# Kernel tuning notes

Measured on AMD Instinct MI355X. Metric: run time of the kernel, lower is better.

The kernel has to match this reference:

```python
import jax, jax.numpy as jnp
import numpy as np

NUM_CLASSES = 80
TOPK = 9
EPS_OVERLAPS = 1e-6  # mmdet BboxOverlaps2D: union clamped to eps
EPS_YOLOV6 = 1e-9    # yolov6_iou_calculator: eps added to union


def _pairwise_iou(b1, b2, eps, add_eps):
    # b1: (..., M, 4), b2: (..., N, 4) xyxy -> (..., M, N)
    lt = jnp.maximum(b1[..., :, None, :2], b2[..., None, :, :2])
    rb = jnp.minimum(b1[..., :, None, 2:], b2[..., None, :, 2:])
    wh = jnp.clip(rb - lt, 0.0)
    overlap = wh[..., 0] * wh[..., 1]
    a1 = (b1[..., 2] - b1[..., 0]) * (b1[..., 3] - b1[..., 1])
    a2 = (b2[..., 2] - b2[..., 0]) * (b2[..., 3] - b2[..., 1])
    union = a1[..., :, None] + a2[..., None, :] - overlap
    return overlap / (union + eps) if add_eps else overlap / jnp.maximum(union, eps)


def _assign(pred_bboxes, priors, gt_labels, gt_bboxes, pad_bbox_flag, num_level_priors):
    num_level_priors = tuple(int(n) for n in np.asarray(num_level_priors))
    # priors (x, y, stride_w, stride_h) -> 5*stride cell boxes in xyxy
    cell_half = priors[:, 2:] * 2.5
    prior_boxes = jnp.concatenate([priors[:, :2] - cell_half, priors[:, :2] + cell_half], axis=-1)
    bs, num_gt = gt_bboxes.shape[0], gt_bboxes.shape[1]
    num_priors = priors.shape[0]
    gt_flat = gt_bboxes.reshape(-1, 4)

    # step 1: IoU between all priors and all gts
    overlaps = _pairwise_iou(gt_flat, prior_boxes, EPS_OVERLAPS, False).reshape(bs, num_gt, num_priors)

    # step 2: center distances
    gt_cxy = (gt_flat[:, :2] + gt_flat[:, 2:]) * 0.5
    prior_cxy = (prior_boxes[:, :2] + prior_boxes[:, 2:]) * 0.5
    dist = jnp.sqrt(jnp.sum((gt_cxy[:, None, :] - prior_cxy[None, :, :]) ** 2, axis=-1))
    dist = dist.reshape(bs, num_gt, num_priors)

    # step 3: per-level topk closest candidates
    pad_bool = pad_bbox_flag[..., 0] > 0  # (bs, num_gt)
    b_ix = jnp.arange(bs)[:, None, None]
    g_ix = jnp.arange(num_gt)[None, :, None]
    is_in_list, cand_list = [], []
    start = 0
    for pl in num_level_priors:
        k = min(TOPK, pl)
        d_l = jax.lax.dynamic_slice_in_dim(dist, start, pl, axis=-1)
        _, idx = jax.lax.top_k(-d_l, k)  # (bs, num_gt, k) smallest distances
        cand_list.append(idx + start)
        idx_m = jnp.where(pad_bool[..., None], idx, 0)
        counts = jnp.zeros((bs, num_gt, pl), dist.dtype).at[b_ix, g_ix, idx_m].add(1.0)
        is_in_list.append(jnp.where(counts > 1, jnp.zeros_like(counts), counts))
        start += pl
    is_in_candidate = jnp.concatenate(is_in_list, axis=-1)   # (bs, num_gt, num_priors)
    candidate_idxs = jnp.concatenate(cand_list, axis=-1)     # (bs, num_gt, k*levels)

    # step 4: mean + std of candidate IoUs as threshold
    candidate_overlaps = jnp.where(is_in_candidate > 0, overlaps, jnp.zeros_like(overlaps))
    gathered = jnp.take_along_axis(candidate_overlaps, candidate_idxs, axis=-1)
    thr = jnp.mean(gathered, axis=-1, keepdims=True) + jnp.std(gathered, axis=-1, keepdims=True, ddof=1)

    # step 5: keep candidates above threshold
    is_pos = jnp.where(candidate_overlaps > thr, is_in_candidate, jnp.zeros_like(is_in_candidate))

    # step 6: center of prior must lie inside gt box
    lt = prior_cxy[None, None, :, :] - gt_bboxes[:, :, None, :2]
    rb = gt_bboxes[:, :, None, 2:] - prior_cxy[None, None, :, :]
    is_in_gts = (jnp.minimum(lt, rb).min(axis=-1) > 1e-9).astype(gt_bboxes.dtype)

    pos_mask = is_pos * is_in_gts * pad_bbox_flag  # pad flag broadcasts (bs,num_gt,1)

    # resolve priors assigned to multiple gts: keep highest IoU gt
    fg = pos_mask.sum(axis=-2)  # (bs, num_priors)
    best_gt = jnp.argmax(overlaps, axis=1)  # (bs, num_priors)
    is_max = jax.nn.one_hot(best_gt, num_gt, dtype=pos_mask.dtype).transpose(0, 2, 1)
    pos_mask = jnp.where(fg[:, None, :] > 1, is_max, pos_mask)
    fg_mask = pos_mask.sum(axis=-2)                 # (bs, num_priors)
    gt_idx = jnp.argmax(pos_mask, axis=-2)          # (bs, num_priors)

    # targets
    flat_idx = gt_idx + jnp.arange(bs)[:, None] * num_gt
    assigned_labels = gt_labels.reshape(-1)[flat_idx]
    assigned_labels = jnp.where(fg_mask > 0, assigned_labels, NUM_CLASSES)
    assigned_bboxes = gt_bboxes.reshape(-1, 4)[flat_idx]
    assigned_scores = jax.nn.one_hot(assigned_labels, NUM_CLASSES + 1, dtype=gt_bboxes.dtype)[..., :NUM_CLASSES]

    # weight scores by IoU with predictions
    ious = _pairwise_iou(gt_bboxes, pred_bboxes, EPS_YOLOV6, True) * pos_mask
    assigned_scores = assigned_scores * jnp.max(ious, axis=-2)[..., None]
    return assigned_labels, assigned_bboxes, assigned_scores, fg_mask > 0


def setup_inputs() -> dict:
    key = jax.random.key(0)
    k0, k1, k2, k3, k4 = jax.random.split(key, 5)
    bs, num_gt, img = 32, 64, 640
    strides = (8, 16, 32)
    pri = []
    for s in strides:
        n = img // s
        xs = (np.arange(n, dtype=np.float32) + 0.5) * s
        gy, gx = np.meshgrid(xs, xs, indexing='ij')
        pts = np.stack([gx.ravel(), gy.ravel()], axis=1)
        st = np.full((pts.shape[0], 2), s, dtype=np.float32)
        pri.append(np.concatenate([pts, st], axis=1))
    priors = jnp.asarray(np.concatenate(pri, axis=0))  # (8400, 4)
    num_level_priors = (6400, 1600, 400)
    num_priors = priors.shape[0]
    cxy = jax.random.uniform(k0, (bs, num_gt, 2), minval=50.0, maxval=590.0)
    wh = jax.random.uniform(k1, (bs, num_gt, 2), minval=20.0, maxval=200.0)
    gt_bboxes = jnp.concatenate([cxy - wh * 0.5, cxy + wh * 0.5], axis=-1)
    gt_labels = jax.random.randint(k2, (bs, num_gt, 1), 0, NUM_CLASSES)
    pad_bbox_flag = jnp.ones((bs, num_gt, 1), jnp.float32)
    pcxy = priors[None, :, :2] + jax.random.normal(k3, (bs, num_priors, 2)) * 4.0
    pwh = jax.random.uniform(k4, (bs, num_priors, 2), minval=10.0, maxval=150.0)
    pred_bboxes = jnp.concatenate([pcxy - pwh * 0.5, pcxy + pwh * 0.5], axis=-1)
    return {'pred_bboxes': pred_bboxes, 'priors': priors, 'gt_labels': gt_labels,
            'gt_bboxes': gt_bboxes, 'pad_bbox_flag': pad_bbox_flag,
            'num_level_priors': num_level_priors}


def reference(pred_bboxes, priors, gt_labels, gt_bboxes, pad_bbox_flag, num_level_priors):
    return _assign(pred_bboxes, priors, gt_labels, gt_bboxes, pad_bbox_flag, num_level_priors)
```

## Files before the change

### kernel.cpp

```cpp
#include <hip/hip_runtime.h>

#define BS 32
#define NG 64
#define NP 8400
#define NTOPK 9
#define NUM_CLASSES 80
#define NCAND 27

__device__ __forceinline__ unsigned long long wave_min_u64(unsigned long long k) {
    #pragma unroll
    for (int off = 1; off < 64; off <<= 1) {
        unsigned long long o = __shfl_xor(k, off, 64);
        k = (o < k) ? o : k;
    }
    return k;
}

__global__ __launch_bounds__(256) void k_candidates(
    const float4* __restrict__ gt_bboxes,
    const float*  __restrict__ pad_flag,
    unsigned long long* __restrict__ posbits
) {
    const int bg   = (blockIdx.x * 256 + threadIdx.x) >> 6;
    const int lane = threadIdx.x & 63;
    const int b  = bg >> 6;
    const int g  = bg & 63;

    const float4 gt  = gt_bboxes[bg];
    const float  pad = pad_flag[bg];
    const float  gcx = (gt.x + gt.z) * 0.5f;
    const float  gcy = (gt.y + gt.w) * 0.5f;
    const float  garea = (gt.z - gt.x) * (gt.w - gt.y);

    const float lvl_s[3] = {8.0f, 16.0f, 32.0f};
    const int   lvl_n[3] = {80, 40, 20};
    const int   lvl_b[3] = {0, 6400, 8000};

    float ov[NCAND];
    int   ixs[NCAND];

    float sum = 0.0f;

    const int dy5 = lane / 5;
    const int dx5 = lane - dy5 * 5;

    #pragma unroll
    for (int L = 0; L < 3; ++L) {
        const float s    = lvl_s[L];
        const int   n    = lvl_n[L];
        const int   base = lvl_b[L];

        int wx = (int)floorf(gcx / s) - 2;
        int wy = (int)floorf(gcy / s) - 2;
        wx = min(max(wx, 0), n - 5);
        wy = min(max(wy, 0), n - 5);

        unsigned long long key = ~0ull;
        if (lane < 25) {
            const int   iy  = wy + dy5;
            const int   ix  = wx + dx5;
            const float py  = ((float)iy + 0.5f) * s;
            const float px  = ((float)ix + 0.5f) * s;
            const float ddx = gcx - px;
            const float ddy = gcy - py;
            const float d   = sqrtf(ddx * ddx + ddy * ddy);
            key = ((unsigned long long)__float_as_uint(d) << 32) |
                  (unsigned int)(base + iy * n + ix);
        }

        const float hx = s * 2.5f;
        #pragma unroll
        for (int q = 0; q < NTOPK; ++q) {
            const unsigned long long m = wave_min_u64(key);
            if (key == m) key = ~0ull;

            const int slot = L * NTOPK + q;
            const int idx  = (int)(m & 0xffffffffu);
            const int rel  = idx - base;
            const int iy   = rel / n;
            const int ix   = rel - iy * n;
            const float px = ((float)ix + 0.5f) * s;
            const float py = ((float)iy + 0.5f) * s;
            const float px0 = px - hx, py0 = py - hx;
            const float px1 = px + hx, py1 = py + hx;
            float lx = fmaxf(gt.x, px0), ly = fmaxf(gt.y, py0);
            float rx = fminf(gt.z, px1), ry = fminf(gt.w, py1);
            float w = fmaxf(rx - lx, 0.0f), h = fmaxf(ry - ly, 0.0f);
            float ovl = w * h;
            float parea = (px1 - px0) * (py1 - py0);
            float o = ovl / fmaxf(garea + parea - ovl, 1e-6f);
            ov[slot]  = o;
            ixs[slot] = idx;
            sum += o;
        }
    }

    const float mean = sum / (float)NCAND;
    float var = 0.0f;
    #pragma unroll
    for (int i = 0; i < NCAND; ++i) {
        float d = ov[i] - mean;
        var += d * d;
    }
    const float thr = mean + sqrtf(var / (float)(NCAND - 1));

    if (pad > 0.0f && lane == 0) {
        #pragma unroll
        for (int i = 0; i < NCAND; ++i) {
            if (ov[i] > thr) {
                const int   L    = i / NTOPK;
                const float s    = lvl_s[L];
                const int   n    = lvl_n[L];
                const int   base = lvl_b[L];
                const int idx = ixs[i];
                const int rel = idx - base;
                const int iy  = rel / n;
                const int ix  = rel - iy * n;
                const float px = ((float)ix + 0.5f) * s;
                const float py = ((float)iy + 0.5f) * s;
                float mm = fminf(fminf(px - gt.x, py - gt.y),
                                 fminf(gt.z - px, gt.w - py));
                if (mm > 1e-9f) {
                    atomicOr(&posbits[(size_t)b * NP + idx], 1ull << g);
                }
            }
        }
    }
}

__global__ __launch_bounds__(256) void k_assign(
    const float4* __restrict__ priors,
    const float4* __restrict__ gt_bboxes,
    const int*    __restrict__ gt_labels,
    const float4* __restrict__ pred_bboxes,
    const unsigned long long* __restrict__ posbits,
    float* __restrict__ out)
{
    __shared__ float4 s_gt[NG];
    __shared__ int    s_lab[NG];
    __shared__ int    s_plab[256];
    __shared__ float  s_piou[256];

    const int b   = blockIdx.y;
    const int tid = threadIdx.x;
    if (tid < NG) {
        s_gt[tid]  = gt_bboxes[b * NG + tid];
        s_lab[tid] = gt_labels[b * NG + tid];
    }
    __syncthreads();

    const int p0 = blockIdx.x * 256;
    const int p  = p0 + tid;
    int   label  = NUM_CLASSES;
    float iou_w  = 0.0f;

    if (p < NP) {
        const size_t bp = (size_t)b * NP + p;
        unsigned long long mask = posbits[bp];
        int fg = __popcll(mask);
        int gidx = 0;

        if (fg > 1) {
            float4 pr = priors[p];
            float hx = pr.z * 2.5f, hy = pr.w * 2.5f;
            float px0 = pr.x - hx, py0 = pr.y - hy, px1 = pr.x + hx, py1 = pr.y + hy;
            float parea = (px1 - px0) * (py1 - py0);
            float best = -1.0f;
            for (int gg = 0; gg < NG; ++gg) {
                float4 gtb = s_gt[gg];
                float lx = fmaxf(gtb.x, px0), ly = fmaxf(gtb.y, py0);
                float rx = fminf(gtb.z, px1), ry = fminf(gtb.w, py1);
                float w = fmaxf(rx - lx, 0.0f), h = fmaxf(ry - ly, 0.0f);
                float ovl = w * h;
                float ga = (gtb.z - gtb.x) * (gtb.w - gtb.y);
                float v = ovl / fmaxf(ga + parea - ovl, 1e-6f);
                if (v > best) { best = v; gidx = gg; }
            }
        } else if (fg == 1) {
            gidx = __ffsll((unsigned long long)mask) - 1;
        }

        const bool  fgm = fg > 0;
        const float4 gtb = s_gt[gidx];
        label = fgm ? s_lab[gidx] : NUM_CLASSES;

        if (fgm) {
            float4 pb = pred_bboxes[bp];
            float lx = fmaxf(gtb.x, pb.x), ly = fmaxf(gtb.y, pb.y);
            float rx = fminf(gtb.z, pb.z), ry = fminf(gtb.w, pb.w);
            float w = fmaxf(rx - lx, 0.0f), h = fmaxf(ry - ly, 0.0f);
            float ov = w * h;
            float ga = (gtb.z - gtb.x) * (gtb.w - gtb.y);
            float pa = (pb.z - pb.x) * (pb.w - pb.y);
            iou_w = ov / (ga + pa - ov + 1e-9f);
        }

        out[bp] = (float)label;
        ((float4*)(out + (size_t)BS * NP))[bp] = gtb;
        out[(size_t)BS * NP * 85 + bp] = fgm ? 1.0f : 0.0f;
    }

    s_plab[tid] = label;
    s_piou[tid] = iou_w;
    __syncthreads();

    const int npr  = min(256, NP - p0);
    const int nfl4 = npr * 20;
    float4* o4 = (float4*)(out + (size_t)BS * NP * 5 + ((size_t)b * NP + p0) * 80);
    for (int q = tid; q < nfl4; q += 256) {
        int pl   = q / 20;
        int comp = q - pl * 20;
        int lab  = s_plab[pl];
        float iw = s_piou[pl];
        int dd = lab - comp * 4;
        float4 v;
        v.x = (dd == 0) ? iw : 0.0f;
        v.y = (dd == 1) ? iw : 0.0f;
        v.z = (dd == 2) ? iw : 0.0f;
        v.w = (dd == 3) ? iw : 0.0f;
        o4[q] = v;
    }
}

extern "C" void kernel_launch(void* const* d_in, const int* in_sizes, int n_in,
                              void* d_out, int out_size, void* d_ws, size_t ws_size,
                              hipStream_t stream) {
    const float4* pred_bboxes = (const float4*)d_in[0];
    const float4* priors      = (const float4*)d_in[1];
    const int*    gt_labels   = (const int*)d_in[2];
    const float4* gt_bboxes   = (const float4*)d_in[3];
    const float*  pad_flag    = (const float*)d_in[4];

    unsigned long long* posbits = (unsigned long long*)d_ws;
    hipMemsetAsync(posbits, 0, (size_t)BS * NP * sizeof(unsigned long long), stream);

    k_candidates<<<dim3(BS * NG * 64 / 256), dim3(256), 0, stream>>>(
        gt_bboxes, pad_flag, posbits);

    k_assign<<<dim3((NP + 255) / 256, BS), dim3(256), 0, stream>>>(
        priors, gt_bboxes, gt_labels, pred_bboxes, posbits, (float*)d_out);
}
```

Before: 129.4 us.

## Zero score tensor with memset and scatter sparse foreground scores via compacted list

The dense 80-class score tensor is no longer written element by element inside the assign kernel. It is cleared with hipMemsetAsync, and the assign kernel appends (index, label, iou) entries for foreground priors to a compacted list through an atomic counter. A new scatter kernel then writes only those nonzero scores. Separately, the candidate top-k reduction now shuffles over only 32 lanes, since just 25 lanes hold valid keys. The aim is to use the DMA/fill path for the large zero write and drop the per-element selects, at the cost of an extra kernel launch, a global atomic, and a second memset.

After: 147.3 us. 13.9% more time.

```diff
diff --git a/kernel.cpp b/kernel.cpp
--- a/kernel.cpp
+++ b/kernel.cpp
@@ -6,10 +6,13 @@
 #define NTOPK 9
 #define NUM_CLASSES 80
 #define NCAND 27
-
-__device__ __forceinline__ unsigned long long wave_min_u64(unsigned long long k) {
+#define MAXENT (BS * NG * NCAND)
+
+#define POSBYTES ((size_t)BS * NP * 8)
+
+__device__ __forceinline__ unsigned long long wave_min_u64_32(unsigned long long k) {
     #pragma unroll
-    for (int off = 1; off < 64; off <<= 1) {
+    for (int off = 1; off < 32; off <<= 1) {
         unsigned long long o = __shfl_xor(k, off, 64);
         k = (o < k) ? o : k;
     }
@@ -71,7 +74,7 @@
         const float hx = s * 2.5f;
         #pragma unroll
         for (int q = 0; q < NTOPK; ++q) {
-            const unsigned long long m = wave_min_u64(key);
+            const unsigned long long m = wave_min_u64_32(key);
             if (key == m) key = ~0ull;
 
             const int slot = L * NTOPK + q;
@@ -134,12 +137,12 @@
     const int*    __restrict__ gt_labels,
     const float4* __restrict__ pred_bboxes,
     const unsigned long long* __restrict__ posbits,
+    unsigned int* __restrict__ counter,
+    uint2*        __restrict__ entries,
     float* __restrict__ out)
 {
     __shared__ float4 s_gt[NG];
     __shared__ int    s_lab[NG];
-    __shared__ int    s_plab[256];
-    __shared__ float  s_piou[256];
 
     const int b   = blockIdx.y;
     const int tid = threadIdx.x;
@@ -149,76 +152,73 @@
     }
     __syncthreads();
 
-    const int p0 = blockIdx.x * 256;
-    const int p  = p0 + tid;
-    int   label  = NUM_CLASSES;
-    float iou_w  = 0.0f;
-
-    if (p < NP) {
-        const size_t bp = (size_t)b * NP + p;
-        unsigned long long mask = posbits[bp];
-        int fg = __popcll(mask);
-        int gidx = 0;
-
-        if (fg > 1) {
-            float4 pr = priors[p];
-            float hx = pr.z * 2.5f, hy = pr.w * 2.5f;
-            float px0 = pr.x - hx, py0 = pr.y - hy, px1 = pr.x + hx, py1 = pr.y + hy;
-            float parea = (px1 - px0) * (py1 - py0);
-            float best = -1.0f;
-            for (int gg = 0; gg < NG; ++gg) {
-                float4 gtb = s_gt[gg];
-                float lx = fmaxf(gtb.x, px0), ly = fmaxf(gtb.y, py0);
-                float rx = fminf(gtb.z, px1), ry = fminf(gtb.w, py1);
-                float w = fmaxf(rx - lx, 0.0f), h = fmaxf(ry - ly, 0.0f);
-                float ovl = w * h;
-                float ga = (gtb.z - gtb.x) * (gtb.w - gtb.y);
-                float v = ovl / fmaxf(ga + parea - ovl, 1e-6f);
-                if (v > best) { best = v; gidx = gg; }
-            }
-        } else if (fg == 1) {
-            gidx = __ffsll((unsigned long long)mask) - 1;
-        }
-
-        const bool  fgm = fg > 0;
-        const float4 gtb = s_gt[gidx];
-        label = fgm ? s_lab[gidx] : NUM_CLASSES;
-
-        if (fgm) {
-            float4 pb = pred_bboxes[bp];
-            float lx = fmaxf(gtb.x, pb.x), ly = fmaxf(gtb.y, pb.y);
-            float rx = fminf(gtb.z, pb.z), ry = fminf(gtb.w, pb.w);
+    const int p = blockIdx.x * 256 + tid;
+    if (p >= NP) return;
+
+    const size_t bp = (size_t)b * NP + p;
+    unsigned long long mask = posbits[bp];
+    int fg = __popcll(mask);
+    int gidx = 0;
+
+    if (fg > 1) {
+        float4 pr = priors[p];
+        float hx = pr.z * 2.5f, hy = pr.w * 2.5f;
+        float px0 = pr.x - hx, py0 = pr.y - hy, px1 = pr.x + hx, py1 = pr.y + hy;
+        float parea = (px1 - px0) * (py1 - py0);
+        float best = -1.0f;
+        for (int gg = 0; gg < NG; ++gg) {
+            float4 gtb = s_gt[gg];
+            float lx = fmaxf(gtb.x, px0), ly = fmaxf(gtb.y, py0);
+            float rx = fminf(gtb.z, px1), ry = fminf(gtb.w, py1);
             float w = fmaxf(rx - lx, 0.0f), h = fmaxf(ry - ly, 0.0f);
-            float ov = w * h;
+            float ovl = w * h;
             float ga = (gtb.z - gtb.x) * (gtb.w - gtb.y);
-            float pa = (pb.z - pb.x) * (pb.w - pb.y);
-            iou_w = ov / (ga + pa - ov + 1e-9f);
-        }
-
-        out[bp] = (float)label;
-        ((float4*)(out + (size_t)BS * NP))[bp] = gtb;
-        out[(size_t)BS * NP * 85 + bp] = fgm ? 1.0f : 0.0f;
-    }
-
-    s_plab[tid] = label;
-    s_piou[tid] = iou_w;
-    __syncthreads();
-
-    const int npr  = min(256, NP - p0);
-    const int nfl4 = npr * 20;
-    float4* o4 = (float4*)(out + (size_t)BS * NP * 5 + ((size_t)b * NP + p0) * 80);
-    for (int q = tid; q < nfl4; q += 256) {
-        int pl   = q / 20;
-        int comp = q - pl * 20;
-        int lab  = s_plab[pl];
-        float iw = s_piou[pl];
-        int dd = lab - comp * 4;
-        float4 v;
-        v.x = (dd == 0) ? iw : 0.0f;
-        v.y = (dd == 1) ? iw : 0.0f;
-        v.z = (dd == 2) ? iw : 0.0f;
-        v.w = (dd == 3) ? iw : 0.0f;
-        o4[q] = v;
+            float v = ovl / fmaxf(ga + parea - ovl, 1e-6f);
+            if (v > best) { best = v; gidx = gg; }
+        }
+    } else if (fg == 1) {
+        gidx = __ffsll((unsigned long long)mask) - 1;
+    }
+
+    const bool   fgm = fg > 0;
+    const float4 gtb = s_gt[gidx];
+    const int  label = fgm ? s_lab[gidx] : NUM_CLASSES;
+
+    out[bp] = (float)label;
+    ((float4*)(out + (size_t)BS * NP))[bp] = gtb;
+    out[(size_t)BS * NP * 85 + bp] = fgm ? 1.0f : 0.0f;
+
+    if (fgm) {
+        float4 pb = pred_bboxes[bp];
+        float lx = fmaxf(gtb.x, pb.x), ly = fmaxf(gtb.y, pb.y);
+        float rx = fminf(gtb.z, pb.z), ry = fminf(gtb.w, pb.w);
+        float w = fmaxf(rx - lx, 0.0f), h = fmaxf(ry - ly, 0.0f);
+        float ov = w * h;
+        float ga = (gtb.z - gtb.x) * (gtb.w - gtb.y);
+        float pa = (pb.z - pb.x) * (pb.w - pb.y);
+        float iou_w = ov / (ga + pa - ov + 1e-9f);
+        unsigned int ei = atomicAdd(counter, 1u);
+        if (ei < (unsigned)MAXENT) {
+            entries[ei] = make_uint2((unsigned)bp * 128u + (unsigned)label,
+                                     __float_as_uint(iou_w));
+        }
+    }
+}
+
+__global__ __launch_bounds__(256) void k_scatter(
+    const unsigned int* __restrict__ counter,
+    const uint2*        __restrict__ entries,
+    float* __restrict__ out)
+{
+    const unsigned int n0 = *counter;
+    const unsigned int n  = n0 < (unsigned)MAXENT ? n0 : (unsigned)MAXENT;
+    float* scores = out + (size_t)BS * NP * 5;
+    for (unsigned int i = blockIdx.x * 256 + threadIdx.x; i < n;
+         i += gridDim.x * 256) {
+        uint2 e = entries[i];
+        unsigned int bp  = e.x >> 7;
+        unsigned int lab = e.x & 127u;
+        scores[(size_t)bp * 80 + lab] = __uint_as_float(e.y);
     }
 }
 
@@ -231,12 +231,22 @@
     const float4* gt_bboxes   = (const float4*)d_in[3];
     const float*  pad_flag    = (const float*)d_in[4];
 
-    unsigned long long* posbits = (unsigned long long*)d_ws;
-    hipMemsetAsync(posbits, 0, (size_t)BS * NP * sizeof(unsigned long long), stream);
+    char* ws = (char*)d_ws;
+    unsigned long long* posbits = (unsigned long long*)ws;
+    unsigned int*       counter = (unsigned int*)(ws + POSBYTES);
+    uint2*              entries = (uint2*)(ws + POSBYTES + 16);
+
+    float* out = (float*)d_out;
+
+    hipMemsetAsync(ws, 0, POSBYTES + 16, stream);
+    hipMemsetAsync(out + (size_t)BS * NP * 5, 0,
+                   (size_t)BS * NP * 80 * sizeof(float), stream);
 
     k_candidates<<<dim3(BS * NG * 64 / 256), dim3(256), 0, stream>>>(
         gt_bboxes, pad_flag, posbits);
 
     k_assign<<<dim3((NP + 255) / 256, BS), dim3(256), 0, stream>>>(
-        priors, gt_bboxes, gt_labels, pred_bboxes, posbits, (float*)d_out);
-}
+        priors, gt_bboxes, gt_labels, pred_bboxes, posbits, counter, entries, out);
+
+    k_scatter<<<dim3(64), dim3(256), 0, stream>>>(counter, entries, out);
+}
```

## Fuse candidate selection with per-prior assignment in per-batch LDS kernel

Applied to the files above, without the earlier changes.

Replaces the memset plus global-atomic candidate kernel with one block per batch that builds the 64-bit positive masks in shared memory. The same block resolves each prior's assigned gt and writes a compact one-byte record. A second kernel expands the records into the full outputs. This drops the memset, the global atomics and the 8-byte mask round trip. The cost is only 32 blocks for the candidate and assignment phase, so most CUs sit idle, and a large 68KB dynamic LDS allocation.

After: 286.2 us. +121.2%, slower.

```diff
diff --git a/kernel.cpp b/kernel.cpp
--- a/kernel.cpp
+++ b/kernel.cpp
@@ -7,156 +7,145 @@
 #define NUM_CLASSES 80
 #define NCAND 27
 
-__device__ __forceinline__ unsigned long long wave_min_u64(unsigned long long k) {
+#define SMEM_A 68480
+
+__device__ __forceinline__ unsigned long long wave_min_u64_32(unsigned long long k) {
     #pragma unroll
-    for (int off = 1; off < 64; off <<= 1) {
+    for (int off = 1; off < 32; off <<= 1) {
         unsigned long long o = __shfl_xor(k, off, 64);
         k = (o < k) ? o : k;
     }
     return k;
 }
 
-__global__ __launch_bounds__(256) void k_candidates(
+__global__ __launch_bounds__(512) void k_batch(
     const float4* __restrict__ gt_bboxes,
     const float*  __restrict__ pad_flag,
-    unsigned long long* __restrict__ posbits
-) {
-    const int bg   = (blockIdx.x * 256 + threadIdx.x) >> 6;
-    const int lane = threadIdx.x & 63;
-    const int b  = bg >> 6;
-    const int g  = bg & 63;
-
-    const float4 gt  = gt_bboxes[bg];
-    const float  pad = pad_flag[bg];
-    const float  gcx = (gt.x + gt.z) * 0.5f;
-    const float  gcy = (gt.y + gt.w) * 0.5f;
-    const float  garea = (gt.z - gt.x) * (gt.w - gt.y);
+    const float4* __restrict__ priors,
+    unsigned char* __restrict__ records)
+{
+    extern __shared__ char smem[];
+    float4*             s_gt   = (float4*)smem;
+    unsigned long long* s_pos  = (unsigned long long*)(smem + 1024);
+    float*              s_padf = (float*)(smem + 1024 + 67200);
+
+    const int tid  = threadIdx.x;
+    const int b    = blockIdx.x;
+    const int lane = tid & 63;
+    const int wv   = tid >> 6;
+
+    for (int i = tid; i < NP; i += 512) s_pos[i] = 0;
+    if (tid < NG) {
+        s_gt[tid]   = gt_bboxes[b * NG + tid];
+        s_padf[tid] = pad_flag[b * NG + tid];
+    }
+    __syncthreads();
 
     const float lvl_s[3] = {8.0f, 16.0f, 32.0f};
     const int   lvl_n[3] = {80, 40, 20};
     const int   lvl_b[3] = {0, 6400, 8000};
-
-    float ov[NCAND];
-    int   ixs[NCAND];
-
-    float sum = 0.0f;
-
-    const int dy5 = lane / 5;
-    const int dx5 = lane - dy5 * 5;
-
-    #pragma unroll
-    for (int L = 0; L < 3; ++L) {
-        const float s    = lvl_s[L];
-        const int   n    = lvl_n[L];
-        const int   base = lvl_b[L];
-
-        int wx = (int)floorf(gcx / s) - 2;
-        int wy = (int)floorf(gcy / s) - 2;
-        wx = min(max(wx, 0), n - 5);
-        wy = min(max(wy, 0), n - 5);
-
-        unsigned long long key = ~0ull;
-        if (lane < 25) {
-            const int   iy  = wy + dy5;
-            const int   ix  = wx + dx5;
-            const float py  = ((float)iy + 0.5f) * s;
-            const float px  = ((float)ix + 0.5f) * s;
-            const float ddx = gcx - px;
-            const float ddy = gcy - py;
-            const float d   = sqrtf(ddx * ddx + ddy * ddy);
-            key = ((unsigned long long)__float_as_uint(d) << 32) |
-                  (unsigned int)(base + iy * n + ix);
-        }
-
-        const float hx = s * 2.5f;
+    const int   dy5 = lane / 5;
+    const int   dx5 = lane - dy5 * 5;
+
+    for (int r = 0; r < 8; ++r) {
+        const int    g   = wv * 8 + r;
+        const float4 gt  = s_gt[g];
+        const float  pad = s_padf[g];
+        const float  gcx = (gt.x + gt.z) * 0.5f;
+        const float  gcy = (gt.y + gt.w) * 0.5f;
+        const float  garea = (gt.z - gt.x) * (gt.w - gt.y);
+
+        float ov[NCAND];
+        int   ixs[NCAND];
+        float sum = 0.0f;
+
         #pragma unroll
-        for (int q = 0; q < NTOPK; ++q) {
-            const unsigned long long m = wave_min_u64(key);
-            if (key == m) key = ~0ull;
-
-            const int slot = L * NTOPK + q;
-            const int idx  = (int)(m & 0xffffffffu);
-            const int rel  = idx - base;
-            const int iy   = rel / n;
-            const int ix   = rel - iy * n;
-            const float px = ((float)ix + 0.5f) * s;
-            const float py = ((float)iy + 0.5f) * s;
-            const float px0 = px - hx, py0 = py - hx;
-            const float px1 = px + hx, py1 = py + hx;
-            float lx = fmaxf(gt.x, px0), ly = fmaxf(gt.y, py0);
-            float rx = fminf(gt.z, px1), ry = fminf(gt.w, py1);
-            float w = fmaxf(rx - lx, 0.0f), h = fmaxf(ry - ly, 0.0f);
-            float ovl = w * h;
-            float parea = (px1 - px0) * (py1 - py0);
-            float o = ovl / fmaxf(garea + parea - ovl, 1e-6f);
-            ov[slot]  = o;
-            ixs[slot] = idx;
-            sum += o;
-        }
-    }
-
-    const float mean = sum / (float)NCAND;
-    float var = 0.0f;
-    #pragma unroll
-    for (int i = 0; i < NCAND; ++i) {
-        float d = ov[i] - mean;
-        var += d * d;
-    }
-    const float thr = mean + sqrtf(var / (float)(NCAND - 1));
-
-    if (pad > 0.0f && lane == 0) {
+        for (int L = 0; L < 3; ++L) {
+            const float s    = lvl_s[L];
+            const int   n    = lvl_n[L];
+            const int   base = lvl_b[L];
+
+            int wx = (int)floorf(gcx / s) - 2;
+            int wy = (int)floorf(gcy / s) - 2;
+            wx = min(max(wx, 0), n - 5);
+            wy = min(max(wy, 0), n - 5);
+
+            unsigned long long key = ~0ull;
+            if (lane < 25) {
+                const int   iy  = wy + dy5;
+                const int   ix  = wx + dx5;
+                const float py  = ((float)iy + 0.5f) * s;
+                const float px  = ((float)ix + 0.5f) * s;
+                const float ddx = gcx - px;
+                const float ddy = gcy - py;
+                const float d   = sqrtf(ddx * ddx + ddy * ddy);
+                key = ((unsigned long long)__float_as_uint(d) << 32) |
+                      (unsigned int)(base + iy * n + ix);
+            }
+
+            const float hx = s * 2.5f;
+            #pragma unroll
+            for (int q = 0; q < NTOPK; ++q) {
+                const unsigned long long m = wave_min_u64_32(key);
+                if (key == m) key = ~0ull;
+
+                const int slot = L * NTOPK + q;
+                const int idx  = (int)(m & 0xffffffffu);
+                const int rel  = idx - base;
+                const int iy   = rel / n;
+                const int ix   = rel - iy * n;
+                const float px = ((float)ix + 0.5f) * s;
+                const float py = ((float)iy + 0.5f) * s;
+                const float px0 = px - hx, py0 = py - hx;
+                const float px1 = px + hx, py1 = py + hx;
+                float lx = fmaxf(gt.x, px0), ly = fmaxf(gt.y, py0);
+                float rx = fminf(gt.z, px1), ry = fminf(gt.w, py1);
+                float w = fmaxf(rx - lx, 0.0f), h = fmaxf(ry - ly, 0.0f);
+                float ovl = w * h;
+                float parea = (px1 - px0) * (py1 - py0);
+                float o = ovl / fmaxf(garea + parea - ovl, 1e-6f);
+                ov[slot]  = o;
+                ixs[slot] = idx;
+                sum += o;
+            }
+        }
+
+        const float mean = sum / (float)NCAND;
+        float var = 0.0f;
         #pragma unroll
         for (int i = 0; i < NCAND; ++i) {
-            if (ov[i] > thr) {
-                const int   L    = i / NTOPK;
-                const float s    = lvl_s[L];
-                const int   n    = lvl_n[L];
-                const int   base = lvl_b[L];
-                const int idx = ixs[i];
-                const int rel = idx - base;
-                const int iy  = rel / n;
-                const int ix  = rel - iy * n;
-                const float px = ((float)ix + 0.5f) * s;
-                const float py = ((float)iy + 0.5f) * s;
-                float mm = fminf(fminf(px - gt.x, py - gt.y),
-                                 fminf(gt.z - px, gt.w - py));
-                if (mm > 1e-9f) {
-                    atomicOr(&posbits[(size_t)b * NP + idx], 1ull << g);
+            float d = ov[i] - mean;
+            var += d * d;
+        }
+        const float thr = mean + sqrtf(var / (float)(NCAND - 1));
+
+        if (pad > 0.0f && lane == 0) {
+            #pragma unroll
+            for (int i = 0; i < NCAND; ++i) {
+                if (ov[i] > thr) {
+                    const int   L    = i / NTOPK;
+                    const float s    = lvl_s[L];
+                    const int   n    = lvl_n[L];
+                    const int   base = lvl_b[L];
+                    const int idx = ixs[i];
+                    const int rel = idx - base;
+                    const int iy  = rel / n;
+                    const int ix  = rel - iy * n;
+                    const float px = ((float)ix + 0.5f) * s;
+                    const float py = ((float)iy + 0.5f) * s;
+                    float mm = fminf(fminf(px - gt.x, py - gt.y),
+                                     fminf(gt.z - px, gt.w - py));
+                    if (mm > 1e-9f) {
+                        atomicOr(&s_pos[idx], 1ull << g);
+                    }
                 }
             }
         }
     }
-}
-
-__global__ __launch_bounds__(256) void k_assign(
-    const float4* __restrict__ priors,
-    const float4* __restrict__ gt_bboxes,
-    const int*    __restrict__ gt_labels,
-    const float4* __restrict__ pred_bboxes,
-    const unsigned long long* __restrict__ posbits,
-    float* __restrict__ out)
-{
-    __shared__ float4 s_gt[NG];
-    __shared__ int    s_lab[NG];
-    __shared__ int    s_plab[256];
-    __shared__ float  s_piou[256];
-
-    const int b   = blockIdx.y;
-    const int tid = threadIdx.x;
-    if (tid < NG) {
-        s_gt[tid]  = gt_bboxes[b * NG + tid];
-        s_lab[tid] = gt_labels[b * NG + tid];
-    }
-    __syncthreads();
-
-    const int p0 = blockIdx.x * 256;
-    const int p  = p0 + tid;
-    int   label  = NUM_CLASSES;
-    float iou_w  = 0.0f;
-
-    if (p < NP) {
-        const size_t bp = (size_t)b * NP + p;
-        unsigned long long mask = posbits[bp];
+    __syncthreads();
+
+    for (int p = tid; p < NP; p += 512) {
+        unsigned long long mask = s_pos[p];
         int fg = __popcll(mask);
         int gidx = 0;
 
@@ -180,7 +169,42 @@
             gidx = __ffsll((unsigned long long)mask) - 1;
         }
 
-        const bool  fgm = fg > 0;
+        records[(size_t)b * NP + p] =
+            fg > 0 ? (unsigned char)(0x40 | gidx) : (unsigned char)0;
+    }
+}
+
+__global__ __launch_bounds__(256) void k_write(
+    const float4* __restrict__ gt_bboxes,
+    const int*    __restrict__ gt_labels,
+    const float4* __restrict__ pred_bboxes,
+    const unsigned char* __restrict__ records,
+    float* __restrict__ out)
+{
+    __shared__ float4 s_gt[NG];
+    __shared__ int    s_lab[NG];
+    __shared__ int    s_plab[256];
+    __shared__ float  s_piou[256];
+
+    const int b   = blockIdx.y;
+    const int tid = threadIdx.x;
+    if (tid < NG) {
+        s_gt[tid]  = gt_bboxes[b * NG + tid];
+        s_lab[tid] = gt_labels[b * NG + tid];
+    }
+    __syncthreads();
+
+    const int p0 = blockIdx.x * 256;
+    const int p  = p0 + tid;
+    int   label  = NUM_CLASSES;
+    float iou_w  = 0.0f;
+
+    if (p < NP) {
+        const size_t bp = (size_t)b * NP + p;
+        const unsigned char rec = records[bp];
+        const bool fgm  = (rec & 0x40) != 0;
+        const int  gidx = rec & 63;
+
         const float4 gtb = s_gt[gidx];
         label = fgm ? s_lab[gidx] : NUM_CLASSES;
 
@@ -231,12 +255,11 @@
     const float4* gt_bboxes   = (const float4*)d_in[3];
     const float*  pad_flag    = (const float*)d_in[4];
 
-    unsigned long long* posbits = (unsigned long long*)d_ws;
-    hipMemsetAsync(posbits, 0, (size_t)BS * NP * sizeof(unsigned long long), stream);
-
-    k_candidates<<<dim3(BS * NG * 64 / 256), dim3(256), 0, stream>>>(
-        gt_bboxes, pad_flag, posbits);
-
-    k_assign<<<dim3((NP + 255) / 256, BS), dim3(256), 0, stream>>>(
-        priors, gt_bboxes, gt_labels, pred_bboxes, posbits, (float*)d_out);
-}
+    unsigned char* records = (unsigned char*)d_ws;
+
+    k_batch<<<dim3(BS), dim3(512), SMEM_A, stream>>>(
+        gt_bboxes, pad_flag, priors, records);
+
+    k_write<<<dim3((NP + 255) / 256, BS), dim3(256), 0, stream>>>(
+        gt_bboxes, gt_labels, pred_bboxes, records, (float*)d_out);
+}
```

## Split assignment into resolve and write kernels, shrink candidate wave reduction

Applied to the files above, without the earlier changes.

Splits the per-prior assignment kernel into a resolve kernel, which picks the matched ground-truth index and stores a one-byte record, and a write kernel, which emits the large outputs from that record. The aim is to keep the divergent 64-way IoU argmax loop out of the bandwidth-bound output writer. It also narrows the top-k wave reduction to 32 lanes, since only 25 lanes hold keys. The cost is an extra kernel launch and an extra round trip of the records buffer through memory.

Result: slower. 143.2 us (+10.7%).

```diff
diff --git a/kernel.cpp b/kernel.cpp
--- a/kernel.cpp
+++ b/kernel.cpp
@@ -7,9 +7,11 @@
 #define NUM_CLASSES 80
 #define NCAND 27
 
-__device__ __forceinline__ unsigned long long wave_min_u64(unsigned long long k) {
+#define POSBYTES ((size_t)BS * NP * 8)
+
+__device__ __forceinline__ unsigned long long wave_min_u64_32(unsigned long long k) {
     #pragma unroll
-    for (int off = 1; off < 64; off <<= 1) {
+    for (int off = 1; off < 32; off <<= 1) {
         unsigned long long o = __shfl_xor(k, off, 64);
         k = (o < k) ? o : k;
     }
@@ -71,7 +73,7 @@
         const float hx = s * 2.5f;
         #pragma unroll
         for (int q = 0; q < NTOPK; ++q) {
-            const unsigned long long m = wave_min_u64(key);
+            const unsigned long long m = wave_min_u64_32(key);
             if (key == m) key = ~0ull;
 
             const int slot = L * NTOPK + q;
@@ -128,12 +130,54 @@
     }
 }
 
-__global__ __launch_bounds__(256) void k_assign(
+__global__ __launch_bounds__(256) void k_resolve(
     const float4* __restrict__ priors,
+    const float4* __restrict__ gt_bboxes,
+    const unsigned long long* __restrict__ posbits,
+    unsigned char* __restrict__ records)
+{
+    __shared__ float4 s_gt[NG];
+    const int b   = blockIdx.y;
+    const int tid = threadIdx.x;
+    if (tid < NG) s_gt[tid] = gt_bboxes[b * NG + tid];
+    __syncthreads();
+
+    const int p = blockIdx.x * 256 + tid;
+    if (p >= NP) return;
+
+    const size_t bp = (size_t)b * NP + p;
+    unsigned long long mask = posbits[bp];
+    int fg = __popcll(mask);
+    int gidx = 0;
+
+    if (fg > 1) {
+        float4 pr = priors[p];
+        float hx = pr.z * 2.5f, hy = pr.w * 2.5f;
+        float px0 = pr.x - hx, py0 = pr.y - hy, px1 = pr.x + hx, py1 = pr.y + hy;
+        float parea = (px1 - px0) * (py1 - py0);
+        float best = -1.0f;
+        for (int gg = 0; gg < NG; ++gg) {
+            float4 gtb = s_gt[gg];
+            float lx = fmaxf(gtb.x, px0), ly = fmaxf(gtb.y, py0);
+            float rx = fminf(gtb.z, px1), ry = fminf(gtb.w, py1);
+            float w = fmaxf(rx - lx, 0.0f), h = fmaxf(ry - ly, 0.0f);
+            float ovl = w * h;
+            float ga = (gtb.z - gtb.x) * (gtb.w - gtb.y);
+            float v = ovl / fmaxf(ga + parea - ovl, 1e-6f);
+            if (v > best) { best = v; gidx = gg; }
+        }
+    } else if (fg == 1) {
+        gidx = __ffsll((unsigned long long)mask) - 1;
+    }
+
+    records[bp] = fg > 0 ? (unsigned char)(0x40 | gidx) : (unsigned char)0;
+}
+
+__global__ __launch_bounds__(256) void k_write(
     const float4* __restrict__ gt_bboxes,
     const int*    __restrict__ gt_labels,
     const float4* __restrict__ pred_bboxes,
-    const unsigned long long* __restrict__ posbits,
+    const unsigned char* __restrict__ records,
     float* __restrict__ out)
 {
     __shared__ float4 s_gt[NG];
@@ -156,31 +200,10 @@
 
     if (p < NP) {
         const size_t bp = (size_t)b * NP + p;
-        unsigned long long mask = posbits[bp];
-        int fg = __popcll(mask);
-        int gidx = 0;
-
-        if (fg > 1) {
-            float4 pr = priors[p];
-            float hx = pr.z * 2.5f, hy = pr.w * 2.5f;
-            float px0 = pr.x - hx, py0 = pr.y - hy, px1 = pr.x + hx, py1 = pr.y + hy;
-            float parea = (px1 - px0) * (py1 - py0);
-            float best = -1.0f;
-            for (int gg = 0; gg < NG; ++gg) {
-                float4 gtb = s_gt[gg];
-                float lx = fmaxf(gtb.x, px0), ly = fmaxf(gtb.y, py0);
-                float rx = fminf(gtb.z, px1), ry = fminf(gtb.w, py1);
-                float w = fmaxf(rx - lx, 0.0f), h = fmaxf(ry - ly, 0.0f);
-                float ovl = w * h;
-                float ga = (gtb.z - gtb.x) * (gtb.w - gtb.y);
-                float v = ovl / fmaxf(ga + parea - ovl, 1e-6f);
-                if (v > best) { best = v; gidx = gg; }
-            }
-        } else if (fg == 1) {
-            gidx = __ffsll((unsigned long long)mask) - 1;
-        }
-
-        const bool  fgm = fg > 0;
+        const unsigned char rec = records[bp];
+        const bool fgm  = (rec & 0x40) != 0;
+        const int  gidx = rec & 63;
+
         const float4 gtb = s_gt[gidx];
         label = fgm ? s_lab[gidx] : NUM_CLASSES;
 
@@ -231,12 +254,18 @@
     const float4* gt_bboxes   = (const float4*)d_in[3];
     const float*  pad_flag    = (const float*)d_in[4];
 
-    unsigned long long* posbits = (unsigned long long*)d_ws;
-    hipMemsetAsync(posbits, 0, (size_t)BS * NP * sizeof(unsigned long long), stream);
+    char* ws = (char*)d_ws;
+    unsigned long long* posbits = (unsigned long long*)ws;
+    unsigned char*      records = (unsigned char*)(ws + POSBYTES);
+
+    hipMemsetAsync(posbits, 0, POSBYTES, stream);
 
     k_candidates<<<dim3(BS * NG * 64 / 256), dim3(256), 0, stream>>>(
         gt_bboxes, pad_flag, posbits);
 
-    k_assign<<<dim3((NP + 255) / 256, BS), dim3(256), 0, stream>>>(
-        priors, gt_bboxes, gt_labels, pred_bboxes, posbits, (float*)d_out);
-}
+    k_resolve<<<dim3((NP + 255) / 256, BS), dim3(256), 0, stream>>>(
+        priors, gt_bboxes, posbits, records);
+
+    k_write<<<dim3((NP + 255) / 256, BS), dim3(256), 0, stream>>>(
+        gt_bboxes, gt_labels, pred_bboxes, records, (float*)d_out);
+}
```
